# Kernel optimization log

Hardware: AMD Instinct MI355X
Metric: run time of the kernel (lower is better)

Reference implementation:

```python
import jax, jax.numpy as jnp
import numpy as np

RADIUS = 0.2
NSAMPLE = 32
USE_XYZ = True

B, N, S, C = 8, 8192, 2048, 64


def setup_inputs() -> dict:
    key = jax.random.key(0)
    k1, k2, k3 = jax.random.split(key, 3)
    xyz = jax.random.uniform(k1, (B, N, 3), dtype=jnp.float32)
    new_xyz = jax.random.uniform(k2, (B, S, 3), dtype=jnp.float32)
    features = jax.random.normal(k3, (B, N, C), dtype=jnp.float32)
    return {"xyz": xyz, "new_xyz": new_xyz, "features": features}


def _ball_query(new_xyz, xyz, radius, nsample):
    # new_xyz: (B,S,3), xyz: (B,N,3) -> idx (B,S,nsample) int32
    n = xyz.shape[1]
    d2 = jnp.sum((new_xyz[:, :, None, :] - xyz[:, None, :, :]) ** 2, axis=-1)  # (B,S,N)
    mask = d2 < radius * radius
    # keys: index j if inside ball else N (sentinel); smallest nsample keys = first
    # nsample in-ball indices in ascending j order (matches CUDA ball_query order).
    keys = jnp.where(mask, jnp.arange(n, dtype=jnp.int32), jnp.int32(n))
    neg_vals, _ = jax.lax.top_k(-keys, nsample)  # top_k of -keys -> smallest keys
    idx = -neg_vals  # (B,S,nsample), ascending
    first = idx[..., 0:1]
    idx = jnp.where(idx == n, first, idx)   # pad empty slots with first hit
    idx = jnp.where(idx == n, 0, idx)       # balls with zero hits -> index 0
    return idx


def _group(points, idx):
    # points: (B,N,D), idx: (B,S,K) -> (B,S,K,D)
    return jax.vmap(lambda p, i: p[i])(points, idx)


def reference(xyz, new_xyz, features):
    idx = _ball_query(new_xyz, xyz, RADIUS, NSAMPLE)
    grouped_xyz = _group(xyz, idx) - new_xyz[:, :, None, :]  # (B,S,K,3)
    grouped_feat = _group(features, idx)                      # (B,S,K,C)
    if USE_XYZ:
        new_features = jnp.concatenate([grouped_xyz, grouped_feat], axis=-1)
    else:
        new_features = grouped_feat
    return jnp.transpose(new_features, (0, 3, 1, 2))  # (B, C+3, S, K)
```

## Files before the change

### kernel.cpp

```cpp
#include <hip/hip_runtime.h>

#define BB 8
#define NN 8192
#define SS 2048
#define CC 64
#define NS 32
#define COUT 67
#define QT 8
#define P0 19

typedef float f32x4 __attribute__((ext_vector_type(4)));

__global__ __launch_bounds__(256) void scan_kernel(
    const float* __restrict__ xyz,
    const float* __restrict__ new_xyz,
    int* __restrict__ idx_ws)
{
#pragma clang fp contract(off)
    const int wave = threadIdx.x >> 6;
    const int lane = threadIdx.x & 63;
    const int qid  = blockIdx.x * 4 + wave;
    const int b = qid >> 11;
    const int s = qid & 2047;

    const float R2 = 0.04f;

    const float* ctr = new_xyz + ((size_t)b * SS + s) * 3;
    const float cx = ctr[0], cy = ctr[1], cz = ctr[2];
    const float* xb = xyz + (size_t)b * NN * 3;

    int* myidx = idx_ws + (size_t)qid * NS;
    const unsigned long long lt = (1ull << lane) - 1ull;

    int total = 0;
    int firstIdx = -1;
    for (int j0 = 0; j0 < NN && total < NS; j0 += 256) {
        const float4* p4 = (const float4*)(xb + (size_t)(j0 + (lane << 2)) * 3);
        const float4 A  = p4[0];
        const float4 Bv = p4[1];
        const float4 Cv = p4[2];
        float d2v[4];
        {
            const float dx = A.x - cx, dy = A.y - cy, dz = A.z - cz;
            float d2 = dx * dx; d2 = d2 + dy * dy; d2 = d2 + dz * dz;
            d2v[0] = d2;
        }
        {
            const float dx = A.w - cx, dy = Bv.x - cy, dz = Bv.y - cz;
            float d2 = dx * dx; d2 = d2 + dy * dy; d2 = d2 + dz * dz;
            d2v[1] = d2;
        }
        {
            const float dx = Bv.z - cx, dy = Bv.w - cy, dz = Cv.x - cz;
            float d2 = dx * dx; d2 = d2 + dy * dy; d2 = d2 + dz * dz;
            d2v[2] = d2;
        }
        {
            const float dx = Cv.y - cx, dy = Cv.z - cy, dz = Cv.w - cz;
            float d2 = dx * dx; d2 = d2 + dy * dy; d2 = d2 + dz * dz;
            d2v[3] = d2;
        }

        unsigned long long M[4];
#pragma unroll
        for (int u = 0; u < 4; ++u) M[u] = __ballot(d2v[u] < R2);

        if (firstIdx < 0) {
            int fmin = 0x7fffffff;
#pragma unroll
            for (int u = 0; u < 4; ++u)
                if (M[u] != 0ull) {
                    const int j = j0 + (__builtin_ctzll(M[u]) << 2) + u;
                    fmin = (j < fmin) ? j : fmin;
                }
            if (fmin != 0x7fffffff) firstIdx = fmin;
        }

        int below = 0;
#pragma unroll
        for (int u = 0; u < 4; ++u) below += (int)__popcll(M[u] & lt);

        int own = 0;
#pragma unroll
        for (int u = 0; u < 4; ++u) {
            if (d2v[u] < R2) {
                const int pos = total + below + own;
                if (pos < NS) myidx[pos] = j0 + (lane << 2) + u;
                ++own;
            }
        }
#pragma unroll
        for (int u = 0; u < 4; ++u) total += (int)__popcll(M[u]);
    }
    if (total < NS) {
        const int fill = (total > 0) ? firstIdx : 0;
        if (lane >= total && lane < NS) myidx[lane] = fill;
    }
}

__global__ __launch_bounds__(256) void gather_kernel(
    const float* __restrict__ xyz,
    const float* __restrict__ new_xyz,
    const float* __restrict__ feat,
    const int* __restrict__ idx_ws,
    float* __restrict__ out)
{
#pragma clang fp contract(off)
    __shared__ float tile[P0 * QT * NS];
    __shared__ int idx_sh[QT * NS];

    const int t   = threadIdx.x;
    const int bid = blockIdx.x;
    const int b     = bid & 7;
    const int rem   = bid >> 3;
    const int quad  = rem & 3;
    const int sTile = rem >> 2;

    const int s0 = sTile * QT;
    const int qbase = (b << 11) + s0;

    idx_sh[t] = idx_ws[(size_t)qbase * NS + t];
    __syncthreads();

    const int q = t >> 5;
    const int row = idx_sh[t];

    const float* frow = feat + ((size_t)b * NN + row) * CC + quad * 16;
    const int pb = (quad == 0) ? 3 : 0;
    if (quad == 0) {
        const float* ctr = new_xyz + ((size_t)b * SS + s0 + q) * 3;
        const float* p   = xyz + ((size_t)b * NN + row) * 3;
        tile[0 * 256 + t] = p[0] - ctr[0];
        tile[1 * 256 + t] = p[1] - ctr[1];
        tile[2 * 256 + t] = p[2] - ctr[2];
    }
#pragma unroll
    for (int i = 0; i < 4; ++i) {
        const float4 f = *(const float4*)(frow + i * 4);
        tile[(pb + i * 4 + 0) * 256 + t] = f.x;
        tile[(pb + i * 4 + 1) * 256 + t] = f.y;
        tile[(pb + i * 4 + 2) * 256 + t] = f.z;
        tile[(pb + i * 4 + 3) * 256 + t] = f.w;
    }
    __syncthreads();

    const int P     = (quad == 0) ? P0 : 16;
    const int cbase = (quad == 0) ? 0 : (3 + quad * 16);
    const int wv = t >> 6;
    const int ln = t & 63;
    const size_t plane = (size_t)SS * NS;
    float* ob = out + (((size_t)b * COUT + cbase) * SS + s0) * NS;
#pragma unroll
    for (int i = 0; i < 5; ++i) {
        const int p = i * 4 + wv;
        if (p < P) {
            const f32x4 v = *(const f32x4*)(tile + p * 256 + ln * 4);
            __builtin_nontemporal_store(v, (f32x4*)(ob + (size_t)p * plane + ln * 4));
        }
    }
}

extern "C" void kernel_launch(void* const* d_in, const int* in_sizes, int n_in,
                              void* d_out, int out_size, void* d_ws, size_t ws_size,
                              hipStream_t stream) {
    const float* xyz     = (const float*)d_in[0];
    const float* new_xyz = (const float*)d_in[1];
    const float* feat    = (const float*)d_in[2];
    float* out = (float*)d_out;
    int* idx_ws = (int*)d_ws;

    scan_kernel<<<dim3((BB * SS) / 4), dim3(256), 0, stream>>>(xyz, new_xyz, idx_ws);
    gather_kernel<<<dim3(SS / QT * 4 * BB), dim3(256), 0, stream>>>(xyz, new_xyz, feat, idx_ws, out);
}
```

Before: 198.3 us.

## Restructure gather to load full feature rows per block with padded LDS transpose

The gather kernel now has each block handle 4 queries and all 67 output channels, instead of splitting channels into quarters over 8 queries. Each wave reads whole 256-byte feature rows coalesced, one lane per channel, and stores them into a padded (stride 65) shared tile to avoid bank conflicts. The transpose is then written out as scalar nontemporal stores of 128 contiguous floats per channel plane. Global reads become fully coalesced and redundant index loads disappear. In exchange the output stores shrink from float4 to scalar width, and each block now writes 512-byte runs per plane instead of 1 KB.

```diff
diff --git a/kernel.cpp b/kernel.cpp
--- a/kernel.cpp
+++ b/kernel.cpp
@@ -6,8 +6,9 @@
 #define CC 64
 #define NS 32
 #define COUT 67
-#define QT 8
-#define P0 19
+#define QT 4
+#define SLOTS (QT*NS)
+#define FSTR 65
 
 typedef float f32x4 __attribute__((ext_vector_type(4)));
 
@@ -106,56 +107,59 @@
     float* __restrict__ out)
 {
 #pragma clang fp contract(off)
-    __shared__ float tile[P0 * QT * NS];
-    __shared__ int idx_sh[QT * NS];
+    __shared__ float ft[SLOTS * FSTR];
+    __shared__ float xt[3 * SLOTS];
+    __shared__ int idx_sh[SLOTS];
 
     const int t   = threadIdx.x;
     const int bid = blockIdx.x;
     const int b     = bid & 7;
-    const int rem   = bid >> 3;
-    const int quad  = rem & 3;
-    const int sTile = rem >> 2;
-
+    const int sTile = bid >> 3;
     const int s0 = sTile * QT;
     const int qbase = (b << 11) + s0;
 
-    idx_sh[t] = idx_ws[(size_t)qbase * NS + t];
+    if (t < SLOTS) idx_sh[t] = idx_ws[(size_t)qbase * NS + t];
     __syncthreads();
 
-    const int q = t >> 5;
-    const int row = idx_sh[t];
+    if (t < SLOTS) {
+        const int r = idx_sh[t];
+        const int q = t >> 5;
+        const float* ctr = new_xyz + ((size_t)b * SS + s0 + q) * 3;
+        const float* p   = xyz + ((size_t)b * NN + r) * 3;
+        xt[0 * SLOTS + t] = p[0] - ctr[0];
+        xt[1 * SLOTS + t] = p[1] - ctr[1];
+        xt[2 * SLOTS + t] = p[2] - ctr[2];
+    }
 
-    const float* frow = feat + ((size_t)b * NN + row) * CC + quad * 16;
-    const int pb = (quad == 0) ? 3 : 0;
-    if (quad == 0) {
-        const float* ctr = new_xyz + ((size_t)b * SS + s0 + q) * 3;
-        const float* p   = xyz + ((size_t)b * NN + row) * 3;
-        tile[0 * 256 + t] = p[0] - ctr[0];
-        tile[1 * 256 + t] = p[1] - ctr[1];
-        tile[2 * 256 + t] = p[2] - ctr[2];
-    }
+    const int w  = t >> 6;
+    const int ln = t & 63;
+    const float* fb = feat + (size_t)b * NN * CC;
+    for (int i = 0; i < 32; i += 4) {
+        float v[4];
+        int   mm[4];
 #pragma unroll
-    for (int i = 0; i < 4; ++i) {
-        const float4 f = *(const float4*)(frow + i * 4);
-        tile[(pb + i * 4 + 0) * 256 + t] = f.x;
-        tile[(pb + i * 4 + 1) * 256 + t] = f.y;
-        tile[(pb + i * 4 + 2) * 256 + t] = f.z;
-        tile[(pb + i * 4 + 3) * 256 + t] = f.w;
+        for (int u = 0; u < 4; ++u) {
+            const int m = (w << 5) + i + u;
+            mm[u] = m;
+            v[u]  = fb[(size_t)idx_sh[m] * CC + ln];
+        }
+#pragma unroll
+        for (int u = 0; u < 4; ++u)
+            ft[mm[u] * FSTR + ln] = v[u];
     }
     __syncthreads();
 
-    const int P     = (quad == 0) ? P0 : 16;
-    const int cbase = (quad == 0) ? 0 : (3 + quad * 16);
-    const int wv = t >> 6;
-    const int ln = t & 63;
     const size_t plane = (size_t)SS * NS;
-    float* ob = out + (((size_t)b * COUT + cbase) * SS + s0) * NS;
-#pragma unroll
-    for (int i = 0; i < 5; ++i) {
-        const int p = i * 4 + wv;
-        if (p < P) {
-            const f32x4 v = *(const f32x4*)(tile + p * 256 + ln * 4);
-            __builtin_nontemporal_store(v, (f32x4*)(ob + (size_t)p * plane + ln * 4));
+    float* ob = out + ((size_t)b * COUT * SS + s0) * NS;
+    for (int i = 0; i < 34; ++i) {
+        const int tau = (i << 2) + w;
+        if (tau < 134) {
+            const int p  = tau >> 1;
+            const int j  = tau & 1;
+            const int sl = (j << 6) + ln;
+            const float val = (p < 3) ? xt[p * SLOTS + sl]
+                                      : ft[sl * FSTR + (p - 3)];
+            __builtin_nontemporal_store(val, ob + (size_t)p * plane + sl);
         }
     }
 }
@@ -170,5 +174,5 @@
     int* idx_ws = (int*)d_ws;
 
     scan_kernel<<<dim3((BB * SS) / 4), dim3(256), 0, stream>>>(xyz, new_xyz, idx_ws);
-    gather_kernel<<<dim3(SS / QT * 4 * BB), dim3(256), 0, stream>>>(xyz, new_xyz, feat, idx_ws, out);
+    gather_kernel<<<dim3((BB * SS) / QT), dim3(256), 0, stream>>>(xyz, new_xyz, feat, idx_ws, out);
 }
```

Result: faster. 186.8 us (-5.8%).
